# Kernel optimization log

Hardware: AMD Instinct MI355X
Metric: run time of the kernel (lower is better)

Reference implementation:

```python
import jax, jax.numpy as jnp
import numpy as np


def _log_g(x):
    # log of g(x) where g(x) = relu(x)+0.5 for x>=0 else sigmoid(x)
    return jnp.where(x >= 0, jnp.log(jax.nn.relu(x) + 0.5), -jax.nn.softplus(-x))


def _mingru(inp, h_prev, W, b):
    """Log-space parallel minGRU scan.
    inp: (B,S,Din), h_prev: (B,1,H), W: (2H,Din), b: (2H,) -> (B,S,H)
    """
    gh = jnp.einsum('bsd,ed->bse', inp, W) + b  # (B,S,2H)
    gate, hidden = jnp.split(gh, 2, axis=-1)
    log_coeffs = -jax.nn.softplus(gate)    # log(1 - z_t)
    log_z = -jax.nn.softplus(-gate)        # log z_t
    B, S, H = hidden.shape
    a_star = jnp.concatenate(
        [jnp.zeros((B, 1, H), gate.dtype), jnp.cumsum(log_coeffs, axis=1)], axis=1)  # (B,S+1,H)
    log_values = jnp.concatenate([_log_g(h_prev), log_z + _log_g(hidden)], axis=1)   # (B,S+1,H)
    log_h = a_star + jax.lax.cumlogsumexp(log_values - a_star, axis=1)
    return jnp.exp(log_h)[:, 1:]  # (B,S,H)


def setup_inputs() -> dict:
    key = jax.random.key(0)
    k0, k1, k2 = jax.random.split(key, 3)
    B, S, D, H, L = 8, 2048, 1024, 1024, 4
    x = jax.random.normal(k0, (B, S, D), jnp.float32)
    h = jnp.zeros((L, B, 1, H), jnp.float32)
    W0 = jax.random.normal(k1, (2 * H, D), jnp.float32) * 0.02
    b0 = jnp.zeros((2 * H,), jnp.float32)
    Wl = jax.random.normal(k2, (L - 1, 2 * H, H), jnp.float32) * 0.02
    bl = jnp.zeros((L - 1, 2 * H), jnp.float32)
    return {"x": x, "h": h, "W0": W0, "b0": b0, "Wl": Wl, "bl": bl}


def reference(x, h, W0, b0, Wl, bl):
    num_layers = h.shape[0]
    inp = x
    finals = []
    out = inp
    for lidx in range(num_layers):
        W = W0 if lidx == 0 else Wl[lidx - 1]
        b = b0 if lidx == 0 else bl[lidx - 1]
        out = _mingru(inp, h[lidx], W, b)
        finals.append(out[:, -1:])
        # residual: align is Identity since input_dims == hidden_dims
        out = out + inp
        # dropout == 0.0 -> no mask applied (matches original branch)
        inp = out
    return out, jnp.stack(finals)
```

## Files before the change

### kernel.cpp

```cpp
#include <hip/hip_runtime.h>
#include <hip/hip_bf16.h>

using bf16 = __hip_bfloat16;
typedef __bf16 bf16x8 __attribute__((ext_vector_type(8)));
typedef __bf16 bf16x4 __attribute__((ext_vector_type(4)));
typedef __bf16 bf16x2 __attribute__((ext_vector_type(2)));
typedef float  f32x4  __attribute__((ext_vector_type(4)));

#define B_ 8
#define S_ 2048
#define H_ 1024
#define M_ (B_ * S_)
#define N_ (2 * H_)
#define K_ 1024
#define CHUNKS_ 32
#define CLEN_ 64

__device__ __forceinline__ bf16x8 load8f(const float* p) {
  const float4 a = *(const float4*)p;
  const float4 b = *(const float4*)(p + 4);
  bf16x8 r;
  r[0] = (__bf16)a.x; r[1] = (__bf16)a.y; r[2] = (__bf16)a.z; r[3] = (__bf16)a.w;
  r[4] = (__bf16)b.x; r[5] = (__bf16)b.y; r[6] = (__bf16)b.z; r[7] = (__bf16)b.w;
  return r;
}

__global__ __launch_bounds__(256)
void cvt_f32_bf16(const float* __restrict__ src, bf16* __restrict__ dst, long n) {
  const long i = ((long)blockIdx.x * 256 + threadIdx.x) * 8;
  if (i >= n) return;
  *(bf16x8*)(dst + i) = load8f(src + i);
}

__global__ __launch_bounds__(256)
void cvt_pack_w(const float* __restrict__ src, bf16* __restrict__ dst, int nmat) {
  const long idx = (long)blockIdx.x * 256 + threadIdx.x;
  const long e = idx * 8;
  if (e >= (long)nmat * N_ * K_) return;
  const int m = (int)(e / ((long)N_ * K_));
  const long em = e - (long)m * N_ * K_;
  const int prow = (int)(em >> 10);
  const int col  = (int)(em & (K_ - 1));
  const int g = prow >> 5, ty = (prow >> 4) & 1, u = prow & 15;
  const int orow = ty * H_ + g * 16 + u;
  *(bf16x8*)(dst + ((long)m * N_ + prow) * K_ + col) =
      load8f(src + ((long)m * N_ + orow) * K_ + col);
}

__device__ __forceinline__ float rcpf(float x) { return __builtin_amdgcn_rcpf(x); }

__device__ __forceinline__ void step_coeffs(float gate, float hidden,
                                            float& ca, float& cb) {
  const float e1 = __expf(gate);
  ca = rcpf(1.0f + e1);
  const float z = 1.0f - ca;
  float g;
  if (hidden >= 0.0f) {
    g = hidden + 0.5f;
  } else {
    const float e2 = __expf(hidden);
    g = e2 * rcpf(1.0f + e2);
  }
  cb = z * g;
}

__device__ __forceinline__ float g_of(float x) {
  if (x >= 0.0f) return x + 0.5f;
  const float e = __expf(x);
  return e * rcpf(1.0f + e);
}

#define BK_    64
#define NT_    (K_ / BK_)
#define LBUF_  65536
#define LBOFF_ 32768
#define LHALF_ 16384

__global__ __launch_bounds__(512, 2)
void gemm256(const bf16* __restrict__ A, const bf16* __restrict__ W,
             const float* __restrict__ bias, bf16* __restrict__ C,
             float2* __restrict__ sAB) {
  __shared__ __align__(16) char lds[131072];
  const int tid  = threadIdx.x;
  const int lane = tid & 63;
  const int wv   = tid >> 6;
  const int wm   = wv >> 2;
  const int wn   = wv & 3;
  const int r15  = lane & 15;
  const int kq   = lane >> 4;

  const int flat = blockIdx.x;
  const int sw   = (flat & 7) * 64 + (flat >> 3);
  const int by   = sw >> 3;
  const int bx   = sw & 7;
  const int mBase = by * 256;
  const int nBase = bx * 256;

  size_t srcOff[2];
  int dstOff[2];
#pragma unroll
  for (int q = 0; q < 2; ++q) {
    const int t  = q * 512 + tid;
    const int cc = (t & 7) ^ ((t >> 3) & 7);
    srcOff[q] = (size_t)(t >> 3) * K_ + cc * 8;
    dstOff[q] = q * 8192 + wv * 1024;
  }
  const bf16* aH[2] = {A + (size_t)mBase * K_, A + (size_t)(mBase + 128) * K_};
  const bf16* wH[2] = {W + (size_t)nBase * K_, W + (size_t)(nBase + 128) * K_};

#define STAGE(GB, LOFF)                                                        \
  { _Pragma("unroll") for (int q_ = 0; q_ < 2; ++q_)                           \
      __builtin_amdgcn_global_load_lds(                                        \
          (const __attribute__((address_space(1))) void*)((GB) + srcOff[q_]),  \
          (__attribute__((address_space(3))) void*)(lds + (LOFF) + dstOff[q_]),\
          16, 0, 0); }

  const int xsw  = (r15 & 7) << 4;
  const int col0 = (kq * 16) ^ xsw;
  const int col1 = (64 + kq * 16) ^ xsw;
  const int aRow = wm * LHALF_ + r15 * 128;
  const int bRow = LBOFF_ + (wn >> 1) * LHALF_ + ((wn & 1) * 64 + r15) * 128;

  f32x4 acc[8][4];
#pragma unroll
  for (int i = 0; i < 8; ++i)
#pragma unroll
    for (int j = 0; j < 4; ++j)
#pragma unroll
      for (int r = 0; r < 4; ++r) acc[i][j][r] = 0.0f;

  bf16x8 aF[4][2], bF[4][2];

#define LD_A(BO)                                                               \
  { _Pragma("unroll") for (int i_ = 0; i_ < 4; ++i_) {                         \
      aF[i_][0] = *(const bf16x8*)(lds + (BO) + i_ * 2048 + col0);             \
      aF[i_][1] = *(const bf16x8*)(lds + (BO) + i_ * 2048 + col1); } }

#define LD_B(J0, BO)                                                           \
  { _Pragma("unroll") for (int j_ = 0; j_ < 2; ++j_) {                         \
      bF[(J0) + j_][0] =                                                       \
          *(const bf16x8*)(lds + (BO) + bRow + ((J0) + j_) * 2048 + col0);     \
      bF[(J0) + j_][1] =                                                       \
          *(const bf16x8*)(lds + (BO) + bRow + ((J0) + j_) * 2048 + col1); } }

#define MFMA_Q(I0, J0)                                                         \
  { _Pragma("unroll") for (int i_ = 0; i_ < 4; ++i_)                           \
    _Pragma("unroll") for (int j_ = 0; j_ < 2; ++j_)                           \
    _Pragma("unroll") for (int k_ = 0; k_ < 2; ++k_)                           \
      acc[(I0) + i_][(J0) + j_] = __builtin_amdgcn_mfma_f32_16x16x32_bf16(     \
          aF[i_][k_], bF[(J0) + j_][k_], acc[(I0) + i_][(J0) + j_], 0, 0, 0); }

#define PH_BAR()                                                               \
  __builtin_amdgcn_sched_barrier(0);                                           \
  __builtin_amdgcn_s_barrier();                                                \
  asm volatile("s_waitcnt lgkmcnt(0)" ::: "memory");                           \
  __builtin_amdgcn_sched_barrier(0);                                           \
  __builtin_amdgcn_s_setprio(1);

#define PH_END()                                                               \
  __builtin_amdgcn_s_setprio(0);                                               \
  __builtin_amdgcn_sched_barrier(0);                                           \
  __builtin_amdgcn_s_barrier();

#define PH_END_VM(N)                                                           \
  __builtin_amdgcn_s_setprio(0);                                               \
  __builtin_amdgcn_sched_barrier(0);                                           \
  asm volatile("s_waitcnt vmcnt(" #N ")" ::: "memory");                        \
  __builtin_amdgcn_s_barrier();

  STAGE(aH[0], 0);
  STAGE(aH[1], LHALF_);
  STAGE(wH[0], LBOFF_);
  STAGE(wH[1], LBOFF_ + LHALF_);
  STAGE(wH[0] + BK_, LBUF_ + LBOFF_);
  STAGE(aH[0] + BK_, LBUF_);
  asm volatile("s_waitcnt vmcnt(4)" ::: "memory");
  __builtin_amdgcn_s_barrier();

#pragma unroll 1
  for (int t = 0; t < NT_ - 2; t += 2) {
    const int o1 = (t + 1) * BK_, o2 = (t + 2) * BK_, o3 = (t + 3) * BK_;
    LD_A(aRow); LD_B(0, 0);
    STAGE(aH[1] + o1, LBUF_ + LHALF_);
    asm volatile("s_waitcnt lgkmcnt(8)" ::: "memory");
    PH_BAR(); MFMA_Q(0, 0); PH_END();
    LD_B(2, 0);
    STAGE(wH[1] + o1, LBUF_ + LBOFF_ + LHALF_);
    PH_BAR(); MFMA_Q(0, 2); PH_END();
    LD_A(aRow + 8192);
    STAGE(wH[0] + o2, LBOFF_);
    PH_BAR(); MFMA_Q(4, 0); PH_END();
    STAGE(aH[0] + o2, 0);
    PH_BAR(); MFMA_Q(4, 2); PH_END_VM(4);
    LD_A(LBUF_ + aRow); LD_B(0, LBUF_);
    STAGE(aH[1] + o2, LHALF_);
    asm volatile("s_waitcnt lgkmcnt(8)" ::: "memory");
    PH_BAR(); MFMA_Q(0, 0); PH_END();
    LD_B(2, LBUF_);
    STAGE(wH[1] + o2, LBOFF_ + LHALF_);
    PH_BAR(); MFMA_Q(0, 2); PH_END();
    LD_A(LBUF_ + aRow + 8192);
    STAGE(wH[0] + o3, LBUF_ + LBOFF_);
    PH_BAR(); MFMA_Q(4, 0); PH_END();
    STAGE(aH[0] + o3, LBUF_);
    PH_BAR(); MFMA_Q(4, 2); PH_END_VM(4);
  }

  {
    const int o1 = (NT_ - 1) * BK_;
    LD_A(aRow); LD_B(0, 0);
    STAGE(aH[1] + o1, LBUF_ + LHALF_);
    asm volatile("s_waitcnt lgkmcnt(8)" ::: "memory");
    PH_BAR(); MFMA_Q(0, 0); PH_END();
    LD_B(2, 0);
    STAGE(wH[1] + o1, LBUF_ + LBOFF_ + LHALF_);
    PH_BAR(); MFMA_Q(0, 2); PH_END();
    LD_A(aRow + 8192);
    PH_BAR(); MFMA_Q(4, 0); PH_END();
    PH_BAR(); MFMA_Q(4, 2); PH_END_VM(0);
    LD_A(LBUF_ + aRow); LD_B(0, LBUF_);
    PH_BAR(); MFMA_Q(0, 0); PH_END();
    LD_B(2, LBUF_);
    PH_BAR(); MFMA_Q(0, 2); PH_END();
    LD_A(LBUF_ + aRow + 8192);
    PH_BAR(); MFMA_Q(4, 0); PH_END();
    PH_BAR(); MFMA_Q(4, 2);
    __builtin_amdgcn_s_setprio(0);
  }

  const int colBase = nBase + wn * 64;
  const int x0 = (colBase >> 1) + r15;
  const int x1 = x0 + 16;
  const float bg0 = bias[x0], bh0 = bias[H_ + x0];
  const float bg1 = bias[x1], bh1 = bias[H_ + x1];

  float segA[2][8], segB[2][8];
#pragma unroll
  for (int i = 0; i < 8; ++i) {
    float A0 = 1.f, B0 = 0.f, A1 = 1.f, B1 = 0.f;
    const size_t rw0 = (size_t)(mBase + wm * 128 + i * 16 + kq * 4) * N_;
#pragma unroll
    for (int r = 0; r < 4; ++r) {
      float ca0, cb0, ca1, cb1;
      step_coeffs(acc[i][0][r] + bg0, acc[i][1][r] + bh0, ca0, cb0);
      step_coeffs(acc[i][2][r] + bg1, acc[i][3][r] + bh1, ca1, cb1);
      const bf16 qa0 = __float2bfloat16(ca0), qb0 = __float2bfloat16(cb0);
      const bf16 qa1 = __float2bfloat16(ca1), qb1 = __float2bfloat16(cb1);
      const size_t rw = rw0 + (size_t)r * N_;
      C[rw + colBase + r15]      = qa0;
      C[rw + colBase + 16 + r15] = qb0;
      C[rw + colBase + 32 + r15] = qa1;
      C[rw + colBase + 48 + r15] = qb1;
      const float fa0 = __bfloat162float(qa0), fb0 = __bfloat162float(qb0);
      const float fa1 = __bfloat162float(qa1), fb1 = __bfloat162float(qb1);
      A0 = fa0 * A0; B0 = fa0 * B0 + fb0;
      A1 = fa1 * A1; B1 = fa1 * B1 + fb1;
    }
    segA[0][i] = A0; segB[0][i] = B0;
    segA[1][i] = A1; segB[1][i] = B1;
  }

#pragma unroll
  for (int ch = 0; ch < 2; ++ch)
#pragma unroll
    for (int i = 0; i < 8; ++i) {
      float A = segA[ch][i], Bv = segB[ch][i];
      {
        const float pA = __shfl_xor(A, 16, 64);
        const float pB = __shfl_xor(Bv, 16, 64);
        Bv = (lane & 16) ? (A * pB + Bv) : (pA * Bv + pB);
        A = A * pA;
      }
      {
        const float pA = __shfl_xor(A, 32, 64);
        const float pB = __shfl_xor(Bv, 32, 64);
        Bv = (lane & 32) ? (A * pB + Bv) : (pA * Bv + pB);
        A = A * pA;
      }
      segA[ch][i] = A; segB[ch][i] = Bv;
    }

  if (kq == 0) {
    const int b_idx = mBase / S_;
    const int j0 = ((mBase % S_) + wm * 128) / 64;
#pragma unroll
    for (int c = 0; c < 2; ++c) {
#pragma unroll
      for (int ch = 0; ch < 2; ++ch) {
        float A = 1.f, Bv = 0.f;
#pragma unroll
        for (int i = 4 * c; i < 4 * c + 4; ++i) {
          A = segA[ch][i] * A;
          Bv = segA[ch][i] * Bv + segB[ch][i];
        }
        const int x = (ch == 0) ? x0 : x1;
        sAB[(size_t)(j0 + c) * (B_ * H_) + b_idx * 1024 + x] =
            make_float2(A, Bv);
      }
    }
  }
#undef STAGE
#undef LD_A
#undef LD_B
#undef MFMA_Q
#undef PH_BAR
#undef PH_END
#undef PH_END_VM
}

__global__ __launch_bounds__(256)
void scan_apply(const bf16* __restrict__ gh, const float2* __restrict__ sAB,
                const float* __restrict__ hprev,
                const float* rin, float* rout, bf16* __restrict__ gout,
                float* __restrict__ finals) {
  const int tx = threadIdx.x, bx = blockIdx.x;
  const int half = bx & 1, b = (bx >> 1) & 7, j = bx >> 4;
  const int h = half * 512 + tx * 2;
  const int c = b * 1024 + h;
  const int pc = h + ((h >> 4) << 4);

  float h0, h1;
  {
    const float2 hp = *(const float2*)(hprev + c);
    h0 = g_of(hp.x); h1 = g_of(hp.y);
  }
  for (int jj = 0; jj < j; ++jj) {
    const float4 ab = *(const float4*)(sAB + (size_t)jj * (B_ * H_) + c);
    h0 = ab.x * h0 + ab.y;
    h1 = ab.z * h1 + ab.w;
  }

  const size_t rbase = ((size_t)(b * S_ + j * CLEN_)) * H_ + h;
  const bf16* gbase = gh + ((size_t)(b * S_ + j * CLEN_)) * N_ + pc;
#pragma unroll 1
  for (int tt = 0; tt < CLEN_; tt += 8) {
    bf16x2 av[8], bv[8];
    float2 rv[8];
#pragma unroll
    for (int u = 0; u < 8; ++u) {
      const size_t t = (size_t)(tt + u);
      av[u] = *(const bf16x2*)(gbase + t * N_);
      bv[u] = *(const bf16x2*)(gbase + t * N_ + 16);
      rv[u] = *(const float2*)(rin + rbase + t * H_);
    }
#pragma unroll
    for (int u = 0; u < 8; ++u) {
      const size_t t = (size_t)(tt + u);
      h0 = (float)av[u][0] * h0 + (float)bv[u][0];
      h1 = (float)av[u][1] * h1 + (float)bv[u][1];
      const float r0 = h0 + rv[u].x;
      const float r1 = h1 + rv[u].y;
      *(float2*)(rout + rbase + t * H_) = make_float2(r0, r1);
      if (gout) {
        bf16x2 o;
        o[0] = (__bf16)r0; o[1] = (__bf16)r1;
        *(bf16x2*)(gout + rbase + t * H_) = o;
      }
    }
  }
  if (j == CHUNKS_ - 1)
    *(float2*)(finals + c) = make_float2(h0, h1);
}

extern "C" void kernel_launch(void* const* d_in, const int* in_sizes, int n_in,
                              void* d_out, int out_size, void* d_ws,
                              size_t ws_size, hipStream_t stream) {
  const float* x  = (const float*)d_in[0];
  const float* h0 = (const float*)d_in[1];
  const float* W0 = (const float*)d_in[2];
  const float* b0 = (const float*)d_in[3];
  const float* Wl = (const float*)d_in[4];
  const float* bl = (const float*)d_in[5];
  float* out    = (float*)d_out;
  float* finals = out + (size_t)M_ * H_;

  char* ws = (char*)d_ws;
  bf16* gh   = (bf16*)ws;
  bf16* bufA = (bf16*)(ws + (64u << 20));

  const bool wide = ws_size >= ((size_t)115 << 20);
  bf16*   wb  = (bf16*)(ws + (96u << 20));
  float2* sAB = (float2*)(ws + ((wide ? 112u : 101u) << 20));

  cvt_f32_bf16<<<dim3(M_ * K_ / 8 / 256), 256, 0, stream>>>(x, bufA, (long)M_ * K_);
  if (wide) {
    cvt_pack_w<<<dim3(N_ * K_ / 8 / 256), 256, 0, stream>>>(W0, wb, 1);
    cvt_pack_w<<<dim3(3 * N_ * K_ / 8 / 256), 256, 0, stream>>>(
        Wl, wb + (size_t)N_ * K_, 3);
  }

  for (int l = 0; l < 4; ++l) {
    const float* Wf = (l == 0) ? W0 : Wl + (size_t)(l - 1) * N_ * K_;
    const float* bi = (l == 0) ? b0 : bl + (size_t)(l - 1) * N_;
    bf16* wl_ptr;
    if (wide) {
      wl_ptr = wb + (size_t)l * N_ * K_;
    } else {
      cvt_pack_w<<<dim3(N_ * K_ / 8 / 256), 256, 0, stream>>>(Wf, wb, 1);
      wl_ptr = wb;
    }
    gemm256<<<dim3(512), 512, 0, stream>>>(bufA, wl_ptr, bi, gh, sAB);
    scan_apply<<<dim3(512), 256, 0, stream>>>(
        gh, sAB, h0 + (size_t)l * B_ * H_, (l == 0) ? x : out, out,
        (l == 3) ? nullptr : bufA, finals + (size_t)l * B_ * H_);
  }
}
```

Baseline: 565.9 us.

## Make GEMM persistent over two tiles and interleave gate/hidden coefficient layout

The GEMM grid is halved so each block computes two 256x256 tiles in sequence. The first loads of the second tile are issued before the first tile's epilogue runs, so those loads overlap the softmax-coefficient computation and stores. The per-step a/b coefficients are now written as interleaved bf16 pairs, which lets scan_apply read them with a single 8-byte load per timestep instead of two scattered 4-byte loads. The cost is that 256 blocks may underfill a 256-CU device at two blocks per CU, and each block now runs serially for longer.

Result: slower. 650.1 us (+14.9%).

```diff
diff --git a/kernel.cpp b/kernel.cpp
--- a/kernel.cpp
+++ b/kernel.cpp
@@ -89,12 +89,8 @@
   const int r15  = lane & 15;
   const int kq   = lane >> 4;
 
-  const int flat = blockIdx.x;
-  const int sw   = (flat & 7) * 64 + (flat >> 3);
-  const int by   = sw >> 3;
-  const int bx   = sw & 7;
-  const int mBase = by * 256;
-  const int nBase = bx * 256;
+  const int xcd = blockIdx.x & 7;
+  const int idx = blockIdx.x >> 3;
 
   size_t srcOff[2];
   int dstOff[2];
@@ -105,8 +101,6 @@
     srcOff[q] = (size_t)(t >> 3) * K_ + cc * 8;
     dstOff[q] = q * 8192 + wv * 1024;
   }
-  const bf16* aH[2] = {A + (size_t)mBase * K_, A + (size_t)(mBase + 128) * K_};
-  const bf16* wH[2] = {W + (size_t)nBase * K_, W + (size_t)(nBase + 128) * K_};
 
 #define STAGE(GB, LOFF)                                                        \
   { _Pragma("unroll") for (int q_ = 0; q_ < 2; ++q_)                           \
@@ -122,13 +116,6 @@
   const int bRow = LBOFF_ + (wn >> 1) * LHALF_ + ((wn & 1) * 64 + r15) * 128;
 
   f32x4 acc[8][4];
-#pragma unroll
-  for (int i = 0; i < 8; ++i)
-#pragma unroll
-    for (int j = 0; j < 4; ++j)
-#pragma unroll
-      for (int r = 0; r < 4; ++r) acc[i][j][r] = 0.0f;
-
   bf16x8 aF[4][2], bF[4][2];
 
 #define LD_A(BO)                                                               \
@@ -168,135 +155,174 @@
   asm volatile("s_waitcnt vmcnt(" #N ")" ::: "memory");                        \
   __builtin_amdgcn_s_barrier();
 
-  STAGE(aH[0], 0);
-  STAGE(aH[1], LHALF_);
-  STAGE(wH[0], LBOFF_);
-  STAGE(wH[1], LBOFF_ + LHALF_);
-  STAGE(wH[0] + BK_, LBUF_ + LBOFF_);
-  STAGE(aH[0] + BK_, LBUF_);
-  asm volatile("s_waitcnt vmcnt(4)" ::: "memory");
-  __builtin_amdgcn_s_barrier();
-
 #pragma unroll 1
-  for (int t = 0; t < NT_ - 2; t += 2) {
-    const int o1 = (t + 1) * BK_, o2 = (t + 2) * BK_, o3 = (t + 3) * BK_;
-    LD_A(aRow); LD_B(0, 0);
-    STAGE(aH[1] + o1, LBUF_ + LHALF_);
-    asm volatile("s_waitcnt lgkmcnt(8)" ::: "memory");
-    PH_BAR(); MFMA_Q(0, 0); PH_END();
-    LD_B(2, 0);
-    STAGE(wH[1] + o1, LBUF_ + LBOFF_ + LHALF_);
-    PH_BAR(); MFMA_Q(0, 2); PH_END();
-    LD_A(aRow + 8192);
-    STAGE(wH[0] + o2, LBOFF_);
-    PH_BAR(); MFMA_Q(4, 0); PH_END();
-    STAGE(aH[0] + o2, 0);
-    PH_BAR(); MFMA_Q(4, 2); PH_END_VM(4);
-    LD_A(LBUF_ + aRow); LD_B(0, LBUF_);
-    STAGE(aH[1] + o2, LHALF_);
-    asm volatile("s_waitcnt lgkmcnt(8)" ::: "memory");
-    PH_BAR(); MFMA_Q(0, 0); PH_END();
-    LD_B(2, LBUF_);
-    STAGE(wH[1] + o2, LBOFF_ + LHALF_);
-    PH_BAR(); MFMA_Q(0, 2); PH_END();
-    LD_A(LBUF_ + aRow + 8192);
-    STAGE(wH[0] + o3, LBUF_ + LBOFF_);
-    PH_BAR(); MFMA_Q(4, 0); PH_END();
-    STAGE(aH[0] + o3, LBUF_);
-    PH_BAR(); MFMA_Q(4, 2); PH_END_VM(4);
-  }
-
-  {
-    const int o1 = (NT_ - 1) * BK_;
-    LD_A(aRow); LD_B(0, 0);
-    STAGE(aH[1] + o1, LBUF_ + LHALF_);
-    asm volatile("s_waitcnt lgkmcnt(8)" ::: "memory");
-    PH_BAR(); MFMA_Q(0, 0); PH_END();
-    LD_B(2, 0);
-    STAGE(wH[1] + o1, LBUF_ + LBOFF_ + LHALF_);
-    PH_BAR(); MFMA_Q(0, 2); PH_END();
-    LD_A(aRow + 8192);
-    PH_BAR(); MFMA_Q(4, 0); PH_END();
-    PH_BAR(); MFMA_Q(4, 2); PH_END_VM(0);
-    LD_A(LBUF_ + aRow); LD_B(0, LBUF_);
-    PH_BAR(); MFMA_Q(0, 0); PH_END();
-    LD_B(2, LBUF_);
-    PH_BAR(); MFMA_Q(0, 2); PH_END();
-    LD_A(LBUF_ + aRow + 8192);
-    PH_BAR(); MFMA_Q(4, 0); PH_END();
-    PH_BAR(); MFMA_Q(4, 2);
-    __builtin_amdgcn_s_setprio(0);
-  }
-
-  const int colBase = nBase + wn * 64;
-  const int x0 = (colBase >> 1) + r15;
-  const int x1 = x0 + 16;
-  const float bg0 = bias[x0], bh0 = bias[H_ + x0];
-  const float bg1 = bias[x1], bh1 = bias[H_ + x1];
-
-  float segA[2][8], segB[2][8];
-#pragma unroll
-  for (int i = 0; i < 8; ++i) {
-    float A0 = 1.f, B0 = 0.f, A1 = 1.f, B1 = 0.f;
-    const size_t rw0 = (size_t)(mBase + wm * 128 + i * 16 + kq * 4) * N_;
-#pragma unroll
-    for (int r = 0; r < 4; ++r) {
-      float ca0, cb0, ca1, cb1;
-      step_coeffs(acc[i][0][r] + bg0, acc[i][1][r] + bh0, ca0, cb0);
-      step_coeffs(acc[i][2][r] + bg1, acc[i][3][r] + bh1, ca1, cb1);
-      const bf16 qa0 = __float2bfloat16(ca0), qb0 = __float2bfloat16(cb0);
-      const bf16 qa1 = __float2bfloat16(ca1), qb1 = __float2bfloat16(cb1);
-      const size_t rw = rw0 + (size_t)r * N_;
-      C[rw + colBase + r15]      = qa0;
-      C[rw + colBase + 16 + r15] = qb0;
-      C[rw + colBase + 32 + r15] = qa1;
-      C[rw + colBase + 48 + r15] = qb1;
-      const float fa0 = __bfloat162float(qa0), fb0 = __bfloat162float(qb0);
-      const float fa1 = __bfloat162float(qa1), fb1 = __bfloat162float(qb1);
-      A0 = fa0 * A0; B0 = fa0 * B0 + fb0;
-      A1 = fa1 * A1; B1 = fa1 * B1 + fb1;
-    }
-    segA[0][i] = A0; segB[0][i] = B0;
-    segA[1][i] = A1; segB[1][i] = B1;
-  }
-
-#pragma unroll
-  for (int ch = 0; ch < 2; ++ch)
+  for (int tile = 0; tile < 2; ++tile) {
+    const int sw = xcd * 64 + tile * 32 + idx;
+    const int by = sw >> 3;
+    const int bx = sw & 7;
+    const int mBase = by * 256;
+    const int nBase = bx * 256;
+    const bf16* aH[2] = {A + (size_t)mBase * K_, A + (size_t)(mBase + 128) * K_};
+    const bf16* wH[2] = {W + (size_t)nBase * K_, W + (size_t)(nBase + 128) * K_};
+
+    if (tile == 0) {
+      STAGE(aH[0], 0);
+      STAGE(aH[1], LHALF_);
+      STAGE(wH[0], LBOFF_);
+      STAGE(wH[1], LBOFF_ + LHALF_);
+      STAGE(wH[0] + BK_, LBUF_ + LBOFF_);
+      STAGE(aH[0] + BK_, LBUF_);
+      asm volatile("s_waitcnt vmcnt(4)" ::: "memory");
+      __builtin_amdgcn_s_barrier();
+    }
+
+#pragma unroll
+    for (int i = 0; i < 8; ++i)
+#pragma unroll
+      for (int j = 0; j < 4; ++j)
+#pragma unroll
+        for (int r = 0; r < 4; ++r) acc[i][j][r] = 0.0f;
+
+#pragma unroll 1
+    for (int t = 0; t < NT_ - 2; t += 2) {
+      const int o1 = (t + 1) * BK_, o2 = (t + 2) * BK_, o3 = (t + 3) * BK_;
+      LD_A(aRow); LD_B(0, 0);
+      STAGE(aH[1] + o1, LBUF_ + LHALF_);
+      asm volatile("s_waitcnt lgkmcnt(8)" ::: "memory");
+      PH_BAR(); MFMA_Q(0, 0); PH_END();
+      LD_B(2, 0);
+      STAGE(wH[1] + o1, LBUF_ + LBOFF_ + LHALF_);
+      PH_BAR(); MFMA_Q(0, 2); PH_END();
+      LD_A(aRow + 8192);
+      STAGE(wH[0] + o2, LBOFF_);
+      PH_BAR(); MFMA_Q(4, 0); PH_END();
+      STAGE(aH[0] + o2, 0);
+      PH_BAR(); MFMA_Q(4, 2); PH_END_VM(4);
+      LD_A(LBUF_ + aRow); LD_B(0, LBUF_);
+      STAGE(aH[1] + o2, LHALF_);
+      asm volatile("s_waitcnt lgkmcnt(8)" ::: "memory");
+      PH_BAR(); MFMA_Q(0, 0); PH_END();
+      LD_B(2, LBUF_);
+      STAGE(wH[1] + o2, LBOFF_ + LHALF_);
+      PH_BAR(); MFMA_Q(0, 2); PH_END();
+      LD_A(LBUF_ + aRow + 8192);
+      STAGE(wH[0] + o3, LBUF_ + LBOFF_);
+      PH_BAR(); MFMA_Q(4, 0); PH_END();
+      STAGE(aH[0] + o3, LBUF_);
+      PH_BAR(); MFMA_Q(4, 2); PH_END_VM(4);
+    }
+
+    {
+      const int o1 = (NT_ - 1) * BK_;
+      LD_A(aRow); LD_B(0, 0);
+      STAGE(aH[1] + o1, LBUF_ + LHALF_);
+      asm volatile("s_waitcnt lgkmcnt(8)" ::: "memory");
+      PH_BAR(); MFMA_Q(0, 0); PH_END();
+      LD_B(2, 0);
+      STAGE(wH[1] + o1, LBUF_ + LBOFF_ + LHALF_);
+      PH_BAR(); MFMA_Q(0, 2); PH_END();
+      LD_A(aRow + 8192);
+      PH_BAR(); MFMA_Q(4, 0); PH_END();
+      PH_BAR(); MFMA_Q(4, 2); PH_END_VM(0);
+      LD_A(LBUF_ + aRow); LD_B(0, LBUF_);
+      PH_BAR(); MFMA_Q(0, 0); PH_END();
+      LD_B(2, LBUF_);
+      PH_BAR(); MFMA_Q(0, 2); PH_END();
+      LD_A(LBUF_ + aRow + 8192);
+      PH_BAR(); MFMA_Q(4, 0); PH_END();
+      PH_BAR(); MFMA_Q(4, 2);
+      __builtin_amdgcn_s_setprio(0);
+    }
+
+    __builtin_amdgcn_s_barrier();
+
+    if (tile == 0) {
+      const int sw1 = xcd * 64 + 32 + idx;
+      const int m1 = (sw1 >> 3) * 256, n1 = (sw1 & 7) * 256;
+      const bf16* a1[2] = {A + (size_t)m1 * K_, A + (size_t)(m1 + 128) * K_};
+      const bf16* w1[2] = {W + (size_t)n1 * K_, W + (size_t)(n1 + 128) * K_};
+      STAGE(a1[0], 0);
+      STAGE(a1[1], LHALF_);
+      STAGE(w1[0], LBOFF_);
+      STAGE(w1[1], LBOFF_ + LHALF_);
+      STAGE(w1[0] + BK_, LBUF_ + LBOFF_);
+      STAGE(a1[0] + BK_, LBUF_);
+    }
+
+    const int colBase = nBase + wn * 64;
+    const int x0 = (colBase >> 1) + r15;
+    const int x1 = x0 + 16;
+    const float bg0 = bias[x0], bh0 = bias[H_ + x0];
+    const float bg1 = bias[x1], bh1 = bias[H_ + x1];
+
+    float segA[2][8], segB[2][8];
 #pragma unroll
     for (int i = 0; i < 8; ++i) {
-      float A = segA[ch][i], Bv = segB[ch][i];
-      {
-        const float pA = __shfl_xor(A, 16, 64);
-        const float pB = __shfl_xor(Bv, 16, 64);
-        Bv = (lane & 16) ? (A * pB + Bv) : (pA * Bv + pB);
-        A = A * pA;
+      float A0 = 1.f, B0 = 0.f, A1 = 1.f, B1 = 0.f;
+      const size_t rw0 = (size_t)(mBase + wm * 128 + i * 16 + kq * 4) * N_;
+#pragma unroll
+      for (int r = 0; r < 4; ++r) {
+        float ca0, cb0, ca1, cb1;
+        step_coeffs(acc[i][0][r] + bg0, acc[i][1][r] + bh0, ca0, cb0);
+        step_coeffs(acc[i][2][r] + bg1, acc[i][3][r] + bh1, ca1, cb1);
+        bf16x2 p0, p1;
+        p0[0] = (__bf16)ca0; p0[1] = (__bf16)cb0;
+        p1[0] = (__bf16)ca1; p1[1] = (__bf16)cb1;
+        const size_t rw = rw0 + (size_t)r * N_;
+        *(bf16x2*)(C + rw + colBase + 2 * r15)      = p0;
+        *(bf16x2*)(C + rw + colBase + 32 + 2 * r15) = p1;
+        const float fa0 = (float)p0[0], fb0 = (float)p0[1];
+        const float fa1 = (float)p1[0], fb1 = (float)p1[1];
+        A0 = fa0 * A0; B0 = fa0 * B0 + fb0;
+        A1 = fa1 * A1; B1 = fa1 * B1 + fb1;
       }
-      {
-        const float pA = __shfl_xor(A, 32, 64);
-        const float pB = __shfl_xor(Bv, 32, 64);
-        Bv = (lane & 32) ? (A * pB + Bv) : (pA * Bv + pB);
-        A = A * pA;
+      segA[0][i] = A0; segB[0][i] = B0;
+      segA[1][i] = A1; segB[1][i] = B1;
+    }
+
+#pragma unroll
+    for (int ch = 0; ch < 2; ++ch)
+#pragma unroll
+      for (int i = 0; i < 8; ++i) {
+        float Av = segA[ch][i], Bv = segB[ch][i];
+        {
+          const float pA = __shfl_xor(Av, 16, 64);
+          const float pB = __shfl_xor(Bv, 16, 64);
+          Bv = (lane & 16) ? (Av * pB + Bv) : (pA * Bv + pB);
+          Av = Av * pA;
+        }
+        {
+          const float pA = __shfl_xor(Av, 32, 64);
+          const float pB = __shfl_xor(Bv, 32, 64);
+          Bv = (lane & 32) ? (Av * pB + Bv) : (pA * Bv + pB);
+          Av = Av * pA;
+        }
+        segA[ch][i] = Av; segB[ch][i] = Bv;
       }
-      segA[ch][i] = A; segB[ch][i] = Bv;
-    }
-
-  if (kq == 0) {
-    const int b_idx = mBase / S_;
-    const int j0 = ((mBase % S_) + wm * 128) / 64;
-#pragma unroll
-    for (int c = 0; c < 2; ++c) {
-#pragma unroll
-      for (int ch = 0; ch < 2; ++ch) {
-        float A = 1.f, Bv = 0.f;
-#pragma unroll
-        for (int i = 4 * c; i < 4 * c + 4; ++i) {
-          A = segA[ch][i] * A;
-          Bv = segA[ch][i] * Bv + segB[ch][i];
+
+    if (kq == 0) {
+      const int b_idx = mBase / S_;
+      const int j0 = ((mBase % S_) + wm * 128) / 64;
+#pragma unroll
+      for (int c = 0; c < 2; ++c) {
+#pragma unroll
+        for (int ch = 0; ch < 2; ++ch) {
+          float Av = 1.f, Bv = 0.f;
+#pragma unroll
+          for (int i = 4 * c; i < 4 * c + 4; ++i) {
+            Av = segA[ch][i] * Av;
+            Bv = segA[ch][i] * Bv + segB[ch][i];
+          }
+          const int x = (ch == 0) ? x0 : x1;
+          sAB[(size_t)(j0 + c) * (B_ * H_) + b_idx * 1024 + x] =
+              make_float2(Av, Bv);
         }
-        const int x = (ch == 0) ? x0 : x1;
-        sAB[(size_t)(j0 + c) * (B_ * H_) + b_idx * 1024 + x] =
-            make_float2(A, Bv);
       }
+    }
+
+    if (tile == 0) {
+      asm volatile("s_waitcnt vmcnt(0)" ::: "memory");
+      __builtin_amdgcn_s_barrier();
     }
   }
 #undef STAGE
@@ -317,7 +343,6 @@
   const int half = bx & 1, b = (bx >> 1) & 7, j = bx >> 4;
   const int h = half * 512 + tx * 2;
   const int c = b * 1024 + h;
-  const int pc = h + ((h >> 4) << 4);
 
   float h0, h1;
   {
@@ -331,23 +356,22 @@
   }
 
   const size_t rbase = ((size_t)(b * S_ + j * CLEN_)) * H_ + h;
-  const bf16* gbase = gh + ((size_t)(b * S_ + j * CLEN_)) * N_ + pc;
+  const bf16* gbase = gh + ((size_t)(b * S_ + j * CLEN_)) * N_ + 2 * h;
 #pragma unroll 1
   for (int tt = 0; tt < CLEN_; tt += 8) {
-    bf16x2 av[8], bv[8];
+    bf16x4 cv[8];
     float2 rv[8];
 #pragma unroll
     for (int u = 0; u < 8; ++u) {
       const size_t t = (size_t)(tt + u);
-      av[u] = *(const bf16x2*)(gbase + t * N_);
-      bv[u] = *(const bf16x2*)(gbase + t * N_ + 16);
+      cv[u] = *(const bf16x4*)(gbase + t * N_);
       rv[u] = *(const float2*)(rin + rbase + t * H_);
     }
 #pragma unroll
     for (int u = 0; u < 8; ++u) {
       const size_t t = (size_t)(tt + u);
-      h0 = (float)av[u][0] * h0 + (float)bv[u][0];
-      h1 = (float)av[u][1] * h1 + (float)bv[u][1];
+      h0 = (float)cv[u][0] * h0 + (float)cv[u][1];
+      h1 = (float)cv[u][2] * h1 + (float)cv[u][3];
       const float r0 = h0 + rv[u].x;
       const float r1 = h1 + rv[u].y;
       *(float2*)(rout + rbase + t * H_) = make_float2(r0, r1);
@@ -399,7 +423,7 @@
       cvt_pack_w<<<dim3(N_ * K_ / 8 / 256), 256, 0, stream>>>(Wf, wb, 1);
       wl_ptr = wb;
     }
-    gemm256<<<dim3(512), 512, 0, stream>>>(bufA, wl_ptr, bi, gh, sAB);
+    gemm256<<<dim3(256), 512, 0, stream>>>(bufA, wl_ptr, bi, gh, sAB);
     scan_apply<<<dim3(512), 256, 0, stream>>>(
         gh, sAB, h0 + (size_t)l * B_ * H_, (l == 0) ? x : out, out,
         (l == 3) ? nullptr : bufA, finals + (size_t)l * B_ * H_);
```
